# Kernel optimization log

Hardware: AMD Instinct MI355X
Metric: run time of the kernel (lower is better)

## Reference

```python
import jax, jax.numpy as jnp
import numpy as np
import math

NUM_LAYERS = 2
HIDDEN = 512
INPUT = 512  # == HIDDEN so all layer weights stack into [L, H, H]
SEQ = 2048
BATCH = 64


def setup_inputs() -> dict:
    key = jax.random.key(0)
    ks = jax.random.split(key, 8)
    stdv = 1.0 / math.sqrt(HIDDEN)
    u = lambda k, shape: jax.random.uniform(k, shape, jnp.float32, -stdv, stdv)
    x = jax.random.normal(ks[0], (SEQ, BATCH, INPUT), jnp.float32)
    hx = jax.random.normal(ks[1], (NUM_LAYERS, BATCH, HIDDEN), jnp.float32)
    w_ih = u(ks[2], (NUM_LAYERS, HIDDEN, INPUT))   # layer 0: [H, input]; layers>0: [H, H]
    w_hh = u(ks[3], (NUM_LAYERS, HIDDEN, HIDDEN))
    b_ih = u(ks[4], (NUM_LAYERS, HIDDEN))
    b_hh = u(ks[5], (NUM_LAYERS, HIDDEN))
    return {"x": x, "hx": hx, "w_ih": w_ih, "w_hh": w_hh, "b_ih": b_ih, "b_hh": b_hh}


def _rnn_relu(x, hx, w_ih, w_hh, b_ih, b_hh):
    # x: [S, B, I]; hx: [L, B, H]. Standard cuDNN RNN_RELU (seq-major, dropout=0).
    out = x
    h_finals = []
    for l in range(NUM_LAYERS):
        # Hoist the input projection out of the scan: one big GEMM per layer.
        pre = jnp.einsum('sbi,hi->sbh', out, w_ih[l]) + b_ih[l]  # [S, B, H]
        whh_t = w_hh[l].T
        bhh = b_hh[l]

        def step(h, pre_t):
            h_new = jax.nn.relu(pre_t + h @ whh_t + bhh)
            return h_new, h_new

        h_last, out = jax.lax.scan(step, hx[l], pre)
        h_finals.append(h_last)
    return out, jnp.stack(h_finals)  # [S,B,H], [L,B,H]


def reference(x, hx, w_ih, w_hh, b_ih, b_hh):
    return _rnn_relu(x, hx, w_ih, w_hh, b_ih, b_hh)
```

## Files before the change

### kernel.cpp

```cpp
#include <hip/hip_runtime.h>

typedef _Float16 f16;
typedef _Float16 f16x8 __attribute__((ext_vector_type(8)));
typedef float f32x4 __attribute__((ext_vector_type(4)));
typedef unsigned int u32;
typedef u32 u32x4 __attribute__((ext_vector_type(4)));

#define SEQ 2048
#define NBAT 64
#define NH 512
#define OUT0_ELEMS (SEQ * NBAT * NH)
#define TSLICE (NBAT * NH)

#define AGENT __HIP_MEMORY_SCOPE_AGENT
#define RLX __ATOMIC_RELAXED

#define WS_FLAGS 64
#define WS_RING0 8192
#define WS_RING1 (8192 + 4 * 131072)

#define MFMA16(a, b, c) __builtin_amdgcn_mfma_f32_16x16x32_f16((a), (b), (c), 0, 0, 0)

#define WAIT_VM0()                                   \
  do {                                               \
    asm volatile("s_waitcnt vmcnt(0)" ::: "memory"); \
    __builtin_amdgcn_sched_barrier(0);               \
  } while (0)

__device__ __forceinline__ u32x4 ld_sc(const void* p) {
  u32x4 d;
  asm volatile("global_load_dwordx4 %0, %1, off sc0 sc1" : "=v"(d) : "v"(p) : "memory");
  return d;
}
__device__ __forceinline__ void st_sc_u32(void* p, u32 v) {
  asm volatile("global_store_dword %0, %1, off sc0 sc1" ::"v"(p), "v"(v) : "memory");
}
__device__ __forceinline__ void st_sc_u16(void* p, u32 v) {
  asm volatile("global_store_short %0, %1, off sc0 sc1" ::"v"(p), "v"(v) : "memory");
}
__device__ __forceinline__ u32 poll_sc(const void* p) {
  u32 d;
  asm volatile("global_load_dword %0, %1, off sc0 sc1\n\ts_waitcnt vmcnt(0)"
               : "=v"(d) : "v"(p) : "memory");
  return d;
}

__device__ __forceinline__ f16x8 cvt2(float4 a, float4 b) {
  f16x8 v;
  v[0] = (f16)a.x; v[1] = (f16)a.y; v[2] = (f16)a.z; v[3] = (f16)a.w;
  v[4] = (f16)b.x; v[5] = (f16)b.y; v[6] = (f16)b.z; v[7] = (f16)b.w;
  return v;
}
__device__ __forceinline__ f16x8 ldcvt8(const float* p) {
  float4 a = *(const float4*)p;
  float4 b = *(const float4*)(p + 4);
  return cvt2(a, b);
}
__device__ __forceinline__ u32 h2b(float v) {
  union { f16 h[2]; u32 u; } x;
  x.u = 0;
  x.h[0] = (f16)v;
  return x.u;
}

__device__ __forceinline__ bool spin2(const char* fb, u32 tgtA, u32 tgtB, u32* gab) {
  const int lane = threadIdx.x & 63;
  const char* p = fb + lane * 8;
  const u32 tgt = (lane < 32) ? tgtA : tgtB;
  int it = 0;
  for (;;) {
    u32 v = poll_sc(p);
    if (__all((int)(v >= tgt))) return true;
    if (((++it) & 63) == 0) {
      if (__hip_atomic_load(gab, RLX, AGENT) || it > (1 << 20)) {
        __hip_atomic_store(gab, 1u, RLX, AGENT);
        return false;
      }
    }
  }
}

__global__ __launch_bounds__(256) void pre0_gemm(
    const float* __restrict__ x, const float* __restrict__ w_ih,
    const float* __restrict__ b_ih, const float* __restrict__ b_hh,
    float* __restrict__ out) {
  __shared__ __align__(16) char XT[16384];
  const int tid = threadIdx.x;
  const int lane = tid & 63;
  const int wv = tid >> 6;
  const int bid = blockIdx.x;
  const int c = bid >> 8;
  const int r = (bid >> 5) & 7;
  const int ch = bid & 31;
  const int gb = c * 16;
  const int mrow = lane & 15;
  const int kgrp = lane >> 4;
  const int jl = wv * 16 + mrow;
  const int jg = r * 64 + jl;
  const int rsw = (mrow & 7) << 4;

  f16x8 wif[16];
  {
    const float* s1 = w_ih + (size_t)jg * NH + kgrp * 8;
#pragma unroll
    for (int kk = 0; kk < 16; ++kk) wif[kk] = ldcvt8(s1 + kk * 32);
  }
  const float bias = b_ih[jg] + b_hh[jg];
  const f32x4 bias4 = {bias, bias, bias, bias};
  const f32x4 zero4 = {0.f, 0.f, 0.f, 0.f};

  const int sb = tid >> 4;
  const int sk = (tid & 15) * 32;
  const int ssw = (sb & 7) << 4;

#define XA(kk) (*(const f16x8*)(XT + mrow * 1024 + ((((kk) * 64) + kgrp * 16) ^ rsw)))

  for (int ti = 0; ti < 64; ++ti) {
    const int t = ch * 64 + ti;
    {
      const float* sp = x + ((size_t)t * NBAT + gb + sb) * NH + sk;
      float4 a0 = *(const float4*)(sp + 0),  a1 = *(const float4*)(sp + 4);
      float4 a2 = *(const float4*)(sp + 8),  a3 = *(const float4*)(sp + 12);
      float4 a4 = *(const float4*)(sp + 16), a5 = *(const float4*)(sp + 20);
      float4 a6 = *(const float4*)(sp + 24), a7 = *(const float4*)(sp + 28);
      union { f16x8 h; u32x4 u; } v0, v1, v2, v3;
      v0.h = cvt2(a0, a1); v1.h = cvt2(a2, a3);
      v2.h = cvt2(a4, a5); v3.h = cvt2(a6, a7);
      char* d = XT + sb * 1024;
      *(u32x4*)(d + ((sk * 2 + 0) ^ ssw)) = v0.u;
      *(u32x4*)(d + ((sk * 2 + 16) ^ ssw)) = v1.u;
      *(u32x4*)(d + ((sk * 2 + 32) ^ ssw)) = v2.u;
      *(u32x4*)(d + ((sk * 2 + 48) ^ ssw)) = v3.u;
    }
    __syncthreads();
    f32x4 c0 = bias4, c1 = zero4, c2 = zero4, c3 = zero4;
#pragma unroll
    for (int kk = 0; kk < 16; kk += 4) {
      c0 = MFMA16(XA(kk + 0), wif[kk + 0], c0);
      c1 = MFMA16(XA(kk + 1), wif[kk + 1], c1);
      c2 = MFMA16(XA(kk + 2), wif[kk + 2], c2);
      c3 = MFMA16(XA(kk + 3), wif[kk + 3], c3);
    }
    f32x4 acc = (c0 + c1) + (c2 + c3);
    const int fi = ((c * 8 + r) * 4 + wv) * 64 + kgrp * 16 + mrow;
    *(f32x4*)(out + (size_t)t * TSLICE + (size_t)fi * 4) = acc;
    __syncthreads();
  }
#undef XA
}

__global__ __launch_bounds__(256, 1) void rnn_pers(
    const float* __restrict__ x, const float* __restrict__ hx,
    const float* __restrict__ w_ih, const float* __restrict__ w_hh,
    const float* __restrict__ b_ih, const float* __restrict__ b_hh,
    float* __restrict__ out, char* __restrict__ ws) {
  __shared__ __align__(16) char SA[16384];
  __shared__ __align__(16) char SB[16384];
  __shared__ u32 okf;

  const int tid = threadIdx.x;
  const int lane = tid & 63;
  const int wv = tid >> 6;
  const int bid = blockIdx.x;
  const int c = bid >> 4;
  const int layer = (bid >> 3) & 1;
  const int r = bid & 7;

  const int mrow = lane & 15;
  const int kgrp = lane >> 4;
  const int jl = wv * 16 + mrow;
  const int jg = r * 64 + jl;
  const int gb = c * 16;
  const int fq = (r * 4 + wv) * 8;
  const int rsw = (mrow & 7) << 4;

  const int q64 = tid * 64;
  const int ro = tid >> 4;
  const int wb = ro * 1024;
  const int wsw = (ro & 7) << 4;
  const int wc0 = wb + ((((tid & 15) * 64) + 0) ^ wsw);
  const int wc1 = wb + ((((tid & 15) * 64) + 16) ^ wsw);
  const int wc2 = wb + ((((tid & 15) * 64) + 32) ^ wsw);
  const int wc3 = wb + ((((tid & 15) * 64) + 48) ^ wsw);

  u32* gab = (u32*)ws;
  char* fb = ws + WS_FLAGS + c * 512;
  char* ring0 = ws + WS_RING0 + (size_t)c * 131072;
  char* ring1 = ws + WS_RING1 + (size_t)c * 32768;

#define SPIN_OR_DIE(tgA, tgB)                  \
  do {                                         \
    if (wv == 0) {                             \
      bool ok_ = spin2(fb, (tgA), (tgB), gab); \
      if (lane == 0) okf = ok_ ? 1u : 2u;      \
    }                                          \
    __syncthreads();                           \
    if (okf != 1u) return;                     \
  } while (0)

#define LA(kk) (*(const f16x8*)(SA + mrow * 1024 + ((kgrp * 16 + (kk) * 64) ^ rsw)))
#define LB(kk) (*(const f16x8*)(SB + mrow * 1024 + ((kgrp * 16 + (kk) * 64) ^ rsw)))

  f16x8 whf[16];
  {
    const float* s2 = w_hh + ((size_t)layer * NH + jg) * NH + kgrp * 8;
#pragma unroll
    for (int kk = 0; kk < 16; ++kk) whf[kk] = ldcvt8(s2 + kk * 32);
  }
  const f32x4 zero4 = {0.f, 0.f, 0.f, 0.f};

  if (layer == 0) {
    const float* pf =
        out + ((size_t)((c * 8 + r) * 4 + wv) * 64 + kgrp * 16 + mrow) * 4;
    f32x4 xpA = *(const f32x4*)pf;
    f32x4 xpB = *(const f32x4*)(pf + (size_t)TSLICE);
    f32x4 xpC = *(const f32x4*)(pf + (size_t)2 * TSLICE);
    for (int t = 0; t < SEQ; ++t) {
      f32x4 c0 = xpA, c1 = zero4, c2 = zero4, c3 = zero4;
      if (t == 0) {
        const float* hb = hx + (size_t)(gb + mrow) * NH + kgrp * 8;
#pragma unroll
        for (int kk = 0; kk < 16; kk += 4) {
          c0 = MFMA16(ldcvt8(hb + (kk + 0) * 32), whf[kk + 0], c0);
          c1 = MFMA16(ldcvt8(hb + (kk + 1) * 32), whf[kk + 1], c1);
          c2 = MFMA16(ldcvt8(hb + (kk + 2) * 32), whf[kk + 2], c2);
          c3 = MFMA16(ldcvt8(hb + (kk + 3) * 32), whf[kk + 3], c3);
        }
      } else {
        SPIN_OR_DIE((u32)t, (t >= 7) ? (u32)(t - 7) : 0u);
        {
          const char* sp = ring0 + (size_t)((t - 1) & 7) * 16384 + q64;
          u32x4 s0 = ld_sc(sp);
          u32x4 s1 = ld_sc(sp + 16);
          u32x4 s2 = ld_sc(sp + 32);
          u32x4 s3 = ld_sc(sp + 48);
          WAIT_VM0();
          *(u32x4*)(SA + wc0) = s0;
          *(u32x4*)(SA + wc1) = s1;
          *(u32x4*)(SA + wc2) = s2;
          *(u32x4*)(SA + wc3) = s3;
        }
        __syncthreads();
#pragma unroll
        for (int kk = 0; kk < 16; kk += 4) {
          c0 = MFMA16(LA(kk + 0), whf[kk + 0], c0);
          c1 = MFMA16(LA(kk + 1), whf[kk + 1], c1);
          c2 = MFMA16(LA(kk + 2), whf[kk + 2], c2);
          c3 = MFMA16(LA(kk + 3), whf[kk + 3], c3);
        }
      }
      f32x4 acc = (c0 + c1) + (c2 + c3);
      float hv0 = fmaxf(acc[0], 0.f), hv1 = fmaxf(acc[1], 0.f);
      float hv2 = fmaxf(acc[2], 0.f), hv3 = fmaxf(acc[3], 0.f);
      if (t == SEQ - 1) {
        float* hfo = out + OUT0_ELEMS + (size_t)gb * NH + jg;
        hfo[(size_t)(4 * kgrp + 0) * NH] = hv0;
        hfo[(size_t)(4 * kgrp + 1) * NH] = hv1;
        hfo[(size_t)(4 * kgrp + 2) * NH] = hv2;
        hfo[(size_t)(4 * kgrp + 3) * NH] = hv3;
      }
      {
        char* rb = ring0 + (size_t)(t & 7) * 16384 + jg * 2;
        st_sc_u16(rb + (4 * kgrp + 0) * 1024, h2b(hv0));
        st_sc_u16(rb + (4 * kgrp + 1) * 1024, h2b(hv1));
        st_sc_u16(rb + (4 * kgrp + 2) * 1024, h2b(hv2));
        st_sc_u16(rb + (4 * kgrp + 3) * 1024, h2b(hv3));
      }
      WAIT_VM0();
      if (lane == 0) st_sc_u32(fb + fq, (u32)(t + 1));
      xpA = xpB;
      xpB = xpC;
      if (t + 3 < SEQ) xpC = *(const f32x4*)(pf + (size_t)(t + 3) * TSLICE);
    }
  } else {
    f16x8 wif[16];
    {
      const float* s1 = w_ih + ((size_t)NH + jg) * NH + kgrp * 8;
#pragma unroll
      for (int kk = 0; kk < 16; ++kk) wif[kk] = ldcvt8(s1 + kk * 32);
    }
    const float bias = b_ih[NH + jg] + b_hh[NH + jg];
    const f32x4 bias4 = {bias, bias, bias, bias};
    f32x4 xc0, xc1, xc2, xc3;
    SPIN_OR_DIE(1u, 0u);
    {
      const char* sp = ring0 + q64;
      u32x4 s0 = ld_sc(sp);
      u32x4 s1 = ld_sc(sp + 16);
      u32x4 s2 = ld_sc(sp + 32);
      u32x4 s3 = ld_sc(sp + 48);
      WAIT_VM0();
      *(u32x4*)(SB + wc0) = s0;
      *(u32x4*)(SB + wc1) = s1;
      *(u32x4*)(SB + wc2) = s2;
      *(u32x4*)(SB + wc3) = s3;
    }
    __syncthreads();
    xc0 = bias4; xc1 = zero4; xc2 = zero4; xc3 = zero4;
#pragma unroll
    for (int kk = 0; kk < 16; kk += 4) {
      xc0 = MFMA16(LB(kk + 0), wif[kk + 0], xc0);
      xc1 = MFMA16(LB(kk + 1), wif[kk + 1], xc1);
      xc2 = MFMA16(LB(kk + 2), wif[kk + 2], xc2);
      xc3 = MFMA16(LB(kk + 3), wif[kk + 3], xc3);
    }
    for (int t = 0; t < SEQ; ++t) {
      u32 tgtA = (t < SEQ - 1) ? (u32)(t + 2) : (u32)SEQ;
      SPIN_OR_DIE(tgtA, (u32)t);
      {
        u32x4 a0, a1, a2, a3, b0, b1, b2, b3;
        const bool doA = (t >= 1), doB = (t < SEQ - 1);
        if (doA) {
          const char* sp = ring1 + (size_t)((t - 1) & 1) * 16384 + q64;
          a0 = ld_sc(sp); a1 = ld_sc(sp + 16); a2 = ld_sc(sp + 32); a3 = ld_sc(sp + 48);
        }
        if (doB) {
          const char* sp = ring0 + (size_t)((t + 1) & 7) * 16384 + q64;
          b0 = ld_sc(sp); b1 = ld_sc(sp + 16); b2 = ld_sc(sp + 32); b3 = ld_sc(sp + 48);
        }
        WAIT_VM0();
        if (doA) {
          *(u32x4*)(SA + wc0) = a0; *(u32x4*)(SA + wc1) = a1;
          *(u32x4*)(SA + wc2) = a2; *(u32x4*)(SA + wc3) = a3;
        }
        if (doB) {
          *(u32x4*)(SB + wc0) = b0; *(u32x4*)(SB + wc1) = b1;
          *(u32x4*)(SB + wc2) = b2; *(u32x4*)(SB + wc3) = b3;
        }
      }
      __syncthreads();
      f32x4 c0 = xc0, c1 = xc1, c2 = xc2, c3 = xc3;
      if (t == 0) {
        const float* hb = hx + (size_t)(NBAT + gb + mrow) * NH + kgrp * 8;
#pragma unroll
        for (int kk = 0; kk < 16; kk += 4) {
          c0 = MFMA16(ldcvt8(hb + (kk + 0) * 32), whf[kk + 0], c0);
          c1 = MFMA16(ldcvt8(hb + (kk + 1) * 32), whf[kk + 1], c1);
          c2 = MFMA16(ldcvt8(hb + (kk + 2) * 32), whf[kk + 2], c2);
          c3 = MFMA16(ldcvt8(hb + (kk + 3) * 32), whf[kk + 3], c3);
        }
      } else {
#pragma unroll
        for (int kk = 0; kk < 16; kk += 4) {
          c0 = MFMA16(LA(kk + 0), whf[kk + 0], c0);
          c1 = MFMA16(LA(kk + 1), whf[kk + 1], c1);
          c2 = MFMA16(LA(kk + 2), whf[kk + 2], c2);
          c3 = MFMA16(LA(kk + 3), whf[kk + 3], c3);
        }
      }
      f32x4 acc = (c0 + c1) + (c2 + c3);
      float hv0 = fmaxf(acc[0], 0.f), hv1 = fmaxf(acc[1], 0.f);
      float hv2 = fmaxf(acc[2], 0.f), hv3 = fmaxf(acc[3], 0.f);
      if (t == SEQ - 1) {
        float* hfo = out + OUT0_ELEMS + (size_t)(NBAT + gb) * NH + jg;
        hfo[(size_t)(4 * kgrp + 0) * NH] = hv0;
        hfo[(size_t)(4 * kgrp + 1) * NH] = hv1;
        hfo[(size_t)(4 * kgrp + 2) * NH] = hv2;
        hfo[(size_t)(4 * kgrp + 3) * NH] = hv3;
      }
      {
        char* rb = ring1 + (size_t)(t & 1) * 16384 + jg * 2;
        st_sc_u16(rb + (4 * kgrp + 0) * 1024, h2b(hv0));
        st_sc_u16(rb + (4 * kgrp + 1) * 1024, h2b(hv1));
        st_sc_u16(rb + (4 * kgrp + 2) * 1024, h2b(hv2));
        st_sc_u16(rb + (4 * kgrp + 3) * 1024, h2b(hv3));
      }
      WAIT_VM0();
      if (lane == 0) st_sc_u32(fb + 256 + fq, (u32)(t + 1));
      {
        float* ob = out + ((size_t)t * NBAT + gb) * NH + jg;
        ob[(size_t)(4 * kgrp + 0) * NH] = hv0;
        ob[(size_t)(4 * kgrp + 1) * NH] = hv1;
        ob[(size_t)(4 * kgrp + 2) * NH] = hv2;
        ob[(size_t)(4 * kgrp + 3) * NH] = hv3;
      }
      if (t < SEQ - 1) {
        xc0 = bias4; xc1 = zero4; xc2 = zero4; xc3 = zero4;
#pragma unroll
        for (int kk = 0; kk < 16; kk += 4) {
          xc0 = MFMA16(LB(kk + 0), wif[kk + 0], xc0);
          xc1 = MFMA16(LB(kk + 1), wif[kk + 1], xc1);
          xc2 = MFMA16(LB(kk + 2), wif[kk + 2], xc2);
          xc3 = MFMA16(LB(kk + 3), wif[kk + 3], xc3);
        }
      }
    }
  }
#undef LA
#undef LB
#undef SPIN_OR_DIE
}

extern "C" void kernel_launch(void* const* d_in, const int* in_sizes, int n_in,
                              void* d_out, int out_size, void* d_ws, size_t ws_size,
                              hipStream_t stream) {
  (void)in_sizes; (void)n_in; (void)out_size; (void)ws_size;
  const float* x = (const float*)d_in[0];
  const float* hx = (const float*)d_in[1];
  const float* w_ih = (const float*)d_in[2];
  const float* w_hh = (const float*)d_in[3];
  const float* b_ih = (const float*)d_in[4];
  const float* b_hh = (const float*)d_in[5];
  float* out = (float*)d_out;
  char* ws = (char*)d_ws;

  (void)hipMemsetAsync(d_ws, 0, 8192, stream);
  pre0_gemm<<<dim3(1024), dim3(256), 0, stream>>>(x, w_ih, b_ih, b_hh, out);
  rnn_pers<<<dim3(64), dim3(256), 0, stream>>>(x, hx, w_ih, w_hh, b_ih, b_hh, out, ws);
}
```

Measured before the change: 6.603 ms.

## Store layer-0 preactivations as fp16, deepen ring to 16, pack flags

The layer-0 input-projection GEMM now reads x directly into MFMA operands without staging through LDS, uses twice as many blocks with half the timesteps each, and writes its preactivations as fp16 instead of fp32. This halves that intermediate's traffic, and the persistent kernel converts it back to fp32 when it reads it. The layer-0 to layer-1 hidden-state ring grows from 8 to 16 slots so layer 0 can run further ahead of layer 1, and the progress flags are packed at a 4-byte stride instead of 8. Rounding the preactivations to fp16 adds error, and the bigger ring uses more workspace.

Result: slower. 7.652 ms (+15.9%).

```diff
diff --git a/kernel.cpp b/kernel.cpp
--- a/kernel.cpp
+++ b/kernel.cpp
@@ -4,6 +4,7 @@
 typedef _Float16 f16x8 __attribute__((ext_vector_type(8)));
 typedef float f32x4 __attribute__((ext_vector_type(4)));
 typedef unsigned int u32;
+typedef unsigned long long u64;
 typedef u32 u32x4 __attribute__((ext_vector_type(4)));
 
 #define SEQ 2048
@@ -17,7 +18,7 @@
 
 #define WS_FLAGS 64
 #define WS_RING0 8192
-#define WS_RING1 (8192 + 4 * 131072)
+#define WS_RING1 (8192 + 4 * 262144)
 
 #define MFMA16(a, b, c) __builtin_amdgcn_mfma_f32_16x16x32_f16((a), (b), (c), 0, 0, 0)
 
@@ -62,10 +63,18 @@
   x.h[0] = (f16)v;
   return x.u;
 }
+__device__ __forceinline__ f32x4 cvt4(u64 q) {
+  union { u64 q; f16 h[4]; } u;
+  u.q = q;
+  f32x4 r;
+  r[0] = (float)u.h[0]; r[1] = (float)u.h[1];
+  r[2] = (float)u.h[2]; r[3] = (float)u.h[3];
+  return r;
+}
 
 __device__ __forceinline__ bool spin2(const char* fb, u32 tgtA, u32 tgtB, u32* gab) {
   const int lane = threadIdx.x & 63;
-  const char* p = fb + lane * 8;
+  const char* p = fb + lane * 4;
   const u32 tgt = (lane < 32) ? tgtA : tgtB;
   int it = 0;
   for (;;) {
@@ -84,20 +93,18 @@
     const float* __restrict__ x, const float* __restrict__ w_ih,
     const float* __restrict__ b_ih, const float* __restrict__ b_hh,
     float* __restrict__ out) {
-  __shared__ __align__(16) char XT[16384];
   const int tid = threadIdx.x;
   const int lane = tid & 63;
   const int wv = tid >> 6;
   const int bid = blockIdx.x;
-  const int c = bid >> 8;
-  const int r = (bid >> 5) & 7;
-  const int ch = bid & 31;
+  const int c = bid >> 9;
+  const int r = (bid >> 6) & 7;
+  const int ch = bid & 63;
   const int gb = c * 16;
   const int mrow = lane & 15;
   const int kgrp = lane >> 4;
   const int jl = wv * 16 + mrow;
   const int jg = r * 64 + jl;
-  const int rsw = (mrow & 7) << 4;
 
   f16x8 wif[16];
   {
@@ -109,44 +116,26 @@
   const f32x4 bias4 = {bias, bias, bias, bias};
   const f32x4 zero4 = {0.f, 0.f, 0.f, 0.f};
 
-  const int sb = tid >> 4;
-  const int sk = (tid & 15) * 32;
-  const int ssw = (sb & 7) << 4;
-
-#define XA(kk) (*(const f16x8*)(XT + mrow * 1024 + ((((kk) * 64) + kgrp * 16) ^ rsw)))
-
-  for (int ti = 0; ti < 64; ++ti) {
-    const int t = ch * 64 + ti;
-    {
-      const float* sp = x + ((size_t)t * NBAT + gb + sb) * NH + sk;
-      float4 a0 = *(const float4*)(sp + 0),  a1 = *(const float4*)(sp + 4);
-      float4 a2 = *(const float4*)(sp + 8),  a3 = *(const float4*)(sp + 12);
-      float4 a4 = *(const float4*)(sp + 16), a5 = *(const float4*)(sp + 20);
-      float4 a6 = *(const float4*)(sp + 24), a7 = *(const float4*)(sp + 28);
-      union { f16x8 h; u32x4 u; } v0, v1, v2, v3;
-      v0.h = cvt2(a0, a1); v1.h = cvt2(a2, a3);
-      v2.h = cvt2(a4, a5); v3.h = cvt2(a6, a7);
-      char* d = XT + sb * 1024;
-      *(u32x4*)(d + ((sk * 2 + 0) ^ ssw)) = v0.u;
-      *(u32x4*)(d + ((sk * 2 + 16) ^ ssw)) = v1.u;
-      *(u32x4*)(d + ((sk * 2 + 32) ^ ssw)) = v2.u;
-      *(u32x4*)(d + ((sk * 2 + 48) ^ ssw)) = v3.u;
-    }
-    __syncthreads();
+  unsigned short* oh = (unsigned short*)out;
+  const int fi = ((c * 8 + r) * 4 + wv) * 64 + kgrp * 16 + mrow;
+
+  for (int ti = 0; ti < 32; ++ti) {
+    const int t = ch * 32 + ti;
+    const float* xb = x + ((size_t)t * NBAT + gb + mrow) * NH + kgrp * 8;
     f32x4 c0 = bias4, c1 = zero4, c2 = zero4, c3 = zero4;
 #pragma unroll
     for (int kk = 0; kk < 16; kk += 4) {
-      c0 = MFMA16(XA(kk + 0), wif[kk + 0], c0);
-      c1 = MFMA16(XA(kk + 1), wif[kk + 1], c1);
-      c2 = MFMA16(XA(kk + 2), wif[kk + 2], c2);
-      c3 = MFMA16(XA(kk + 3), wif[kk + 3], c3);
+      c0 = MFMA16(ldcvt8(xb + (kk + 0) * 32), wif[kk + 0], c0);
+      c1 = MFMA16(ldcvt8(xb + (kk + 1) * 32), wif[kk + 1], c1);
+      c2 = MFMA16(ldcvt8(xb + (kk + 2) * 32), wif[kk + 2], c2);
+      c3 = MFMA16(ldcvt8(xb + (kk + 3) * 32), wif[kk + 3], c3);
     }
     f32x4 acc = (c0 + c1) + (c2 + c3);
-    const int fi = ((c * 8 + r) * 4 + wv) * 64 + kgrp * 16 + mrow;
-    *(f32x4*)(out + (size_t)t * TSLICE + (size_t)fi * 4) = acc;
-    __syncthreads();
+    union { f16 h[4]; u64 q; } pk;
+    pk.h[0] = (f16)acc[0]; pk.h[1] = (f16)acc[1];
+    pk.h[2] = (f16)acc[2]; pk.h[3] = (f16)acc[3];
+    *(u64*)(oh + (size_t)t * 65536 + (size_t)fi * 4) = pk.q;
   }
-#undef XA
 }
 
 __global__ __launch_bounds__(256, 1) void rnn_pers(
@@ -171,7 +160,7 @@
   const int jl = wv * 16 + mrow;
   const int jg = r * 64 + jl;
   const int gb = c * 16;
-  const int fq = (r * 4 + wv) * 8;
+  const int fq4 = (r * 4 + wv) * 4;
   const int rsw = (mrow & 7) << 4;
 
   const int q64 = tid * 64;
@@ -185,7 +174,7 @@
 
   u32* gab = (u32*)ws;
   char* fb = ws + WS_FLAGS + c * 512;
-  char* ring0 = ws + WS_RING0 + (size_t)c * 131072;
+  char* ring0 = ws + WS_RING0 + (size_t)c * 262144;
   char* ring1 = ws + WS_RING1 + (size_t)c * 32768;
 
 #define SPIN_OR_DIE(tgA, tgB)                  \
@@ -210,13 +199,15 @@
   const f32x4 zero4 = {0.f, 0.f, 0.f, 0.f};
 
   if (layer == 0) {
-    const float* pf =
-        out + ((size_t)((c * 8 + r) * 4 + wv) * 64 + kgrp * 16 + mrow) * 4;
-    f32x4 xpA = *(const f32x4*)pf;
-    f32x4 xpB = *(const f32x4*)(pf + (size_t)TSLICE);
-    f32x4 xpC = *(const f32x4*)(pf + (size_t)2 * TSLICE);
+    const unsigned short* ph =
+        (const unsigned short*)out +
+        (size_t)(((c * 8 + r) * 4 + wv) * 64 + kgrp * 16 + mrow) * 4;
+#define PRE(tt) (*(const u64*)(ph + (size_t)(tt) * 65536))
+    u64 xpA = PRE(0);
+    u64 xpB = PRE(1);
+    u64 xpC = PRE(2);
     for (int t = 0; t < SEQ; ++t) {
-      f32x4 c0 = xpA, c1 = zero4, c2 = zero4, c3 = zero4;
+      f32x4 c0 = cvt4(xpA), c1 = zero4, c2 = zero4, c3 = zero4;
       if (t == 0) {
         const float* hb = hx + (size_t)(gb + mrow) * NH + kgrp * 8;
 #pragma unroll
@@ -227,9 +218,9 @@
           c3 = MFMA16(ldcvt8(hb + (kk + 3) * 32), whf[kk + 3], c3);
         }
       } else {
-        SPIN_OR_DIE((u32)t, (t >= 7) ? (u32)(t - 7) : 0u);
+        SPIN_OR_DIE((u32)t, (t >= 15) ? (u32)(t - 15) : 0u);
         {
-          const char* sp = ring0 + (size_t)((t - 1) & 7) * 16384 + q64;
+          const char* sp = ring0 + (size_t)((t - 1) & 15) * 16384 + q64;
           u32x4 s0 = ld_sc(sp);
           u32x4 s1 = ld_sc(sp + 16);
           u32x4 s2 = ld_sc(sp + 32);
@@ -260,18 +251,19 @@
         hfo[(size_t)(4 * kgrp + 3) * NH] = hv3;
       }
       {
-        char* rb = ring0 + (size_t)(t & 7) * 16384 + jg * 2;
+        char* rb = ring0 + (size_t)(t & 15) * 16384 + jg * 2;
         st_sc_u16(rb + (4 * kgrp + 0) * 1024, h2b(hv0));
         st_sc_u16(rb + (4 * kgrp + 1) * 1024, h2b(hv1));
         st_sc_u16(rb + (4 * kgrp + 2) * 1024, h2b(hv2));
         st_sc_u16(rb + (4 * kgrp + 3) * 1024, h2b(hv3));
       }
       WAIT_VM0();
-      if (lane == 0) st_sc_u32(fb + fq, (u32)(t + 1));
+      if (lane == 0) st_sc_u32(fb + fq4, (u32)(t + 1));
       xpA = xpB;
       xpB = xpC;
-      if (t + 3 < SEQ) xpC = *(const f32x4*)(pf + (size_t)(t + 3) * TSLICE);
-    }
+      if (t + 3 < SEQ) xpC = PRE(t + 3);
+    }
+#undef PRE
   } else {
     f16x8 wif[16];
     {
@@ -315,7 +307,7 @@
           a0 = ld_sc(sp); a1 = ld_sc(sp + 16); a2 = ld_sc(sp + 32); a3 = ld_sc(sp + 48);
         }
         if (doB) {
-          const char* sp = ring0 + (size_t)((t + 1) & 7) * 16384 + q64;
+          const char* sp = ring0 + (size_t)((t + 1) & 15) * 16384 + q64;
           b0 = ld_sc(sp); b1 = ld_sc(sp + 16); b2 = ld_sc(sp + 32); b3 = ld_sc(sp + 48);
         }
         WAIT_VM0();
@@ -366,7 +358,7 @@
         st_sc_u16(rb + (4 * kgrp + 3) * 1024, h2b(hv3));
       }
       WAIT_VM0();
-      if (lane == 0) st_sc_u32(fb + 256 + fq, (u32)(t + 1));
+      if (lane == 0) st_sc_u32(fb + 128 + fq4, (u32)(t + 1));
       {
         float* ob = out + ((size_t)t * NBAT + gb) * NH + jg;
         ob[(size_t)(4 * kgrp + 0) * NH] = hv0;
@@ -405,6 +397,6 @@
   char* ws = (char*)d_ws;
 
   (void)hipMemsetAsync(d_ws, 0, 8192, stream);
-  pre0_gemm<<<dim3(1024), dim3(256), 0, stream>>>(x, w_ih, b_ih, b_hh, out);
+  pre0_gemm<<<dim3(2048), dim3(256), 0, stream>>>(x, w_ih, b_ih, b_hh, out);
   rnn_pers<<<dim3(64), dim3(256), 0, stream>>>(x, hx, w_ih, w_hh, b_ih, b_hh, out, ws);
 }
```
